# Optimization experiments

Measured on AMD Instinct MI355X. Metric: run time of the kernel, lower is better.

## Reference

```python
import jax, jax.numpy as jnp
import numpy as np

# Model dims
P_SPECS = [(6, 256), (7, 256)]          # pattern_length -> num_patterns (ordered)
P = 512                                  # total_num_patterns
MAXL = 7                                 # max_pattern_length
ND = 2                                   # num_diags (self-loop diag + main diag)
D = 300                                  # embedding_dim
V = 50000                                # vocab size
B = 32                                   # batch size
T = 128                                  # max_doc_len
NC = 2                                   # num_classes
NEG = -1e30                              # max-sum semiring zero; one = 0.0
END_STATES = np.concatenate([np.full(n, l - 1, dtype=np.int32) for l, n in P_SPECS])


def setup_inputs() -> dict:
    key = jax.random.key(0)
    ks = jax.random.split(key, 8)
    tokens = jax.random.randint(ks[0], (B, T), 0, V, dtype=jnp.int32)
    doc_lens = jax.random.randint(ks[1], (B,), 64, T + 1, dtype=jnp.int32)
    emb_table = jax.random.normal(ks[2], (V, D), dtype=jnp.float32)
    diags = jax.random.normal(ks[3], (P * ND * MAXL, D), dtype=jnp.float32)
    diags = diags / jnp.linalg.norm(diags, axis=1, keepdims=True)  # normalize(diags)
    bias = jax.random.normal(ks[4], (P * ND * MAXL, 1), dtype=jnp.float32)
    epsilons = jax.random.normal(ks[5], (P, MAXL - 1), dtype=jnp.float32)
    bn_weight = jnp.ones((P,), jnp.float32)
    bn_bias = jnp.zeros((P,), jnp.float32)
    final_w = 0.05 * jax.random.normal(ks[6], (NC, P), dtype=jnp.float32)
    final_b = jnp.zeros((NC,), jnp.float32)
    return dict(tokens=tokens, doc_lens=doc_lens, emb_table=emb_table, diags=diags,
                bias=bias, epsilons=epsilons, bn_weight=bn_weight, bn_bias=bn_bias,
                final_w=final_w, final_b=final_b)


def reference(tokens, doc_lens, emb_table, diags, bias, epsilons,
              bn_weight, bn_bias, final_w, final_b):
    # --- transition matrices (max-sum semiring: from_outer is identity) ---
    emb = emb_table[tokens]                                   # [B,T,D]
    # mm(diags, embeddings) + bias_scale * bias  (bias_scale = 1.0)
    ts = jnp.einsum('btd,kd->btk', emb, diags) + bias[:, 0]   # [B,T,P*ND*MAXL]
    ts = ts.reshape(B, T, P, ND, MAXL)                        # [B,T,P,ND,MAXL]

    end = jnp.asarray(END_STATES)                             # [P]
    hid0 = jnp.full((B, P, MAXL), NEG, jnp.float32).at[:, :, 0].set(0.0)
    sc0 = jnp.full((B, P), NEG, jnp.float32)                  # semiring.zero
    zpad = jnp.full((B, P, 1), NEG, jnp.float32)              # zero_padding
    rpad = jnp.zeros((B, P, 1), jnp.float32)                  # restart_padding (one)

    # epsilon_values = epsilon_scale (one=0) + epsilons
    def step(carry, xs):
        hid, sc = carry
        tm, i = xs                                            # tm: [B,P,ND,MAXL]
        # epsilon transitions
        ae = jnp.maximum(hid, jnp.concatenate([zpad, hid[:, :, :-1] + epsilons], axis=2))
        # main path: diag index -1 (the main diagonal)
        main = jnp.concatenate([rpad, ae[:, :, :-1] + tm[:, :, -1, :-1]], axis=2)
        # self loops: diag 0, self_loop_scale = semiring.one = 0
        sl = ae + tm[:, :, 0, :]
        hid = jnp.maximum(main, sl)
        endv = jnp.take_along_axis(hid, jnp.broadcast_to(end[None, :, None], (B, P, 1)), axis=2)[:, :, 0]
        sc = jnp.where((doc_lens > i)[:, None], jnp.maximum(sc, endv), sc)
        return (hid, sc), None

    (_, scores), _ = jax.lax.scan(step, (hid0, sc0),
                                  (jnp.moveaxis(ts, 1, 0), jnp.arange(T, dtype=jnp.int32)))

    # BatchNorm1d (training mode: biased batch statistics)
    mean = scores.mean(axis=0)
    var = scores.var(axis=0)
    scores = (scores - mean) * jax.lax.rsqrt(var + 1e-5) * bn_weight + bn_bias
    # binarize_scores
    scores = jnp.sign(jax.nn.relu(scores))
    # final linear layer
    return scores @ final_w.T + final_b                       # [B, NC]
```

## Files before the change

kernel.cpp:

```cpp
#include <hip/hip_runtime.h>

#define BB 32
#define TT 128
#define PP 512
#define DD 300
#define KT 10
#define NX 7168
#define AT 256
#define BT 448
#define NEG -1e30f

typedef _Float16 half8 __attribute__((ext_vector_type(8)));
typedef float floatx4 __attribute__((ext_vector_type(4)));

__device__ __forceinline__ void async_load16(const void* g, void* l) {
    __builtin_amdgcn_global_load_lds(
        (const __attribute__((address_space(1))) void*)g,
        (__attribute__((address_space(3))) void*)l, 16, 0, 0);
}

__device__ __forceinline__ floatx4 mfma16(half8 a, half8 b, floatx4 c) {
    return __builtin_amdgcn_mfma_f32_16x16x32_f16(a, b, c, 0, 0, 0);
}

__global__ __launch_bounds__(256) void pack_kernel(
    const int* __restrict__ tokens, const float* __restrict__ emb,
    const float* __restrict__ diags, const float* __restrict__ bias,
    _Float16* __restrict__ AhP, _Float16* __restrict__ AlP,
    _Float16* __restrict__ BhP, _Float16* __restrict__ BlP)
{
    const int idx = blockIdx.x * 256 + threadIdx.x;
    if (idx >= (AT + BT) * KT * 64) return;
    const int chunk = idx >> 6;
    const int ln = idx & 63;

    const float* src;
    float kslot;
    _Float16 *dh, *dl;
    int kt;
    if (chunk < AT * KT) {
        const int mt = chunk / KT; kt = chunk - mt * KT;
        const int m = mt * 16 + (ln & 15);
        src = emb + (size_t)tokens[m] * DD;
        kslot = 1.0f;
        dh = AhP + (size_t)chunk * 512 + ln * 8;
        dl = AlP + (size_t)chunk * 512 + ln * 8;
    } else {
        const int c2 = chunk - AT * KT;
        const int nt = c2 / KT; kt = c2 - nt * KT;
        const int n = nt * 16 + (ln & 15);
        src = diags + (size_t)n * DD;
        kslot = bias[n];
        dh = BhP + (size_t)c2 * 512 + ln * 8;
        dl = BlP + (size_t)c2 * 512 + ln * 8;
    }

    const int k0 = kt * 32 + (ln >> 4) * 8;
    float v[8];
    if (k0 + 8 <= DD) {
        float4 a = *(const float4*)(src + k0);
        float4 b = *(const float4*)(src + k0 + 4);
        v[0] = a.x; v[1] = a.y; v[2] = a.z; v[3] = a.w;
        v[4] = b.x; v[5] = b.y; v[6] = b.z; v[7] = b.w;
    } else {
        #pragma unroll
        for (int i = 0; i < 8; ++i) {
            const int k = k0 + i;
            v[i] = (k < DD) ? src[k] : (k == DD ? kslot : 0.f);
        }
    }
    half8 h, l;
    #pragma unroll
    for (int i = 0; i < 8; ++i) {
        h[i] = (_Float16)v[i];
        l[i] = (_Float16)((v[i] - (float)h[i]) * 4096.f);
    }
    *(half8*)dh = h;
    *(half8*)dl = l;
}

__global__ __launch_bounds__(256, 4) void gemm_kernel(
    const _Float16* __restrict__ AhP, const _Float16* __restrict__ AlP,
    const _Float16* __restrict__ BhP, const _Float16* __restrict__ BlP,
    const int* __restrict__ doc_lens,
    float* __restrict__ C)
{
    __shared__ __align__(16) _Float16 Bs[2][2][8][512];

    const int tid = threadIdx.x;
    const int w = tid >> 6, ln = tid & 63;
    const int n0t = blockIdx.x * 8, m0t = blockIdx.y * 4;
    const int wm = w & 1, wn = w >> 1;

    const int b  = blockIdx.y >> 1;
    const int th = blockIdx.y & 1;
    const int dl = doc_lens[b];
    if (th == 1 && dl <= 64) return;

    floatx4 acc0[2][4], acc1[2][4];
    #pragma unroll
    for (int i = 0; i < 2; ++i)
        #pragma unroll
        for (int j = 0; j < 4; ++j) {
            acc0[i][j] = (floatx4){0.f, 0.f, 0.f, 0.f};
            acc1[i][j] = (floatx4){0.f, 0.f, 0.f, 0.f};
        }

    half8 ah[2][2], al[2][2];

    auto loadA = [&](int kt, int pb) {
        #pragma unroll
        for (int i = 0; i < 2; ++i) {
            const size_t ch = ((size_t)(m0t + wm * 2 + i) * KT + kt) * 512 + ln * 8;
            ah[pb][i] = *(const half8*)(AhP + ch);
            al[pb][i] = *(const half8*)(AlP + ch);
        }
    };
    auto stageB = [&](int kt, int buf) {
        #pragma unroll
        for (int s = 0; s < 2; ++s) {
            const int nt = w + s * 4;
            const size_t ch = ((size_t)(n0t + nt) * KT + kt) * 512 + ln * 8;
            async_load16(BhP + ch, &Bs[buf][0][nt][0]);
            async_load16(BlP + ch, &Bs[buf][1][nt][0]);
        }
    };

    stageB(0, 0);
    loadA(0, 0);
    __syncthreads();

    #pragma unroll
    for (int kt = 0; kt < KT; ++kt) {
        const int cb = kt & 1, nb = cb ^ 1;
        if (kt + 1 < KT) {
            loadA(kt + 1, nb);
            stageB(kt + 1, nb);
        }
        #pragma unroll
        for (int j = 0; j < 4; ++j) {
            const half8 bh = *(const half8*)&Bs[cb][0][wn * 4 + j][ln * 8];
            const half8 bl = *(const half8*)&Bs[cb][1][wn * 4 + j][ln * 8];
            #pragma unroll
            for (int i = 0; i < 2; ++i) {
                acc0[i][j] = mfma16(ah[cb][i], bh, acc0[i][j]);
                acc1[i][j] = mfma16(ah[cb][i], bl, acc1[i][j]);
                acc1[i][j] = mfma16(al[cb][i], bh, acc1[i][j]);
            }
        }
        __syncthreads();
    }

    #pragma unroll
    for (int j = 0; j < 4; ++j) {
        const int n = (n0t + wn * 4 + j) * 16 + (ln & 15);
        #pragma unroll
        for (int i = 0; i < 2; ++i) {
            if (th * 64 + (wm * 2 + i) * 16 < dl) {
                const int mb = (m0t + wm * 2 + i) * 16 + (ln >> 4) * 4;
                #pragma unroll
                for (int r = 0; r < 4; ++r)
                    C[(size_t)(mb + r) * NX + n] =
                        acc0[i][j][r] + acc1[i][j][r] * (1.0f / 4096.0f);
            }
        }
    }
}

__global__ __launch_bounds__(64) void scan_kernel(
    const float* __restrict__ ts,
    const float* __restrict__ epsilons,
    const int* __restrict__ doc_lens,
    float* __restrict__ scores)
{
    const int b = blockIdx.x;
    const int p = blockIdx.y * 64 + threadIdx.x;
    const int dl = doc_lens[b];

    float e[6];
    #pragma unroll
    for (int i = 0; i < 6; ++i) e[i] = epsilons[p * 6 + i];

    const float* base = ts + (size_t)b * TT * NX + p * 14;

    float h0 = 0.f, h1 = NEG, h2 = NEG, h3 = NEG, h4 = NEG, h5 = NEG, h6 = NEG;
    float sc = NEG;
    const bool end5 = (p < 256);

    float2 buf[4][7];

    auto load = [&](int slot, int t) {
        const float2* s = (const float2*)(base + (size_t)t * NX);
        #pragma unroll
        for (int i = 0; i < 7; ++i) buf[slot][i] = s[i];
    };
    auto step = [&](int slot) {
        const float2* v = buf[slot];
        float ae0 = h0;
        float ae1 = fmaxf(h1, h0 + e[0]);
        float ae2 = fmaxf(h2, h1 + e[1]);
        float ae3 = fmaxf(h3, h2 + e[2]);
        float ae4 = fmaxf(h4, h3 + e[3]);
        float ae5 = fmaxf(h5, h4 + e[4]);
        float ae6 = fmaxf(h6, h5 + e[5]);
        h0 = fmaxf(0.f,            ae0 + v[0].x);
        h1 = fmaxf(ae0 + v[3].y,   ae1 + v[0].y);
        h2 = fmaxf(ae1 + v[4].x,   ae2 + v[1].x);
        h3 = fmaxf(ae2 + v[4].y,   ae3 + v[1].y);
        h4 = fmaxf(ae3 + v[5].x,   ae4 + v[2].x);
        h5 = fmaxf(ae4 + v[5].y,   ae5 + v[2].y);
        h6 = fmaxf(ae5 + v[6].x,   ae6 + v[3].x);
        sc = fmaxf(sc, end5 ? h5 : h6);
    };

    #pragma unroll
    for (int j = 0; j < 4; ++j) load(j, j);

    int tb = 0;
    for (; tb + 4 <= dl; tb += 4) {
        #pragma unroll
        for (int j = 0; j < 4; ++j) {
            step(j);
            const int t = tb + j + 4;
            load(j, t > 127 ? 127 : t);
        }
    }
    const int rem = dl - tb;
    #pragma unroll
    for (int j = 0; j < 3; ++j)
        if (j < rem) step(j);

    scores[p * BB + b] = sc;
}

__global__ __launch_bounds__(512) void finalize_kernel(
    const float* __restrict__ scores,
    const float* __restrict__ bn_w,
    const float* __restrict__ bn_b,
    const float* __restrict__ fw,
    const float* __restrict__ fb,
    float* __restrict__ out)
{
    __shared__ float acc[64];
    const int p = threadIdx.x;
    if (p < 64) acc[p] = 0.f;
    __syncthreads();

    float x[32];
    const float4* sp = (const float4*)(scores + p * 32);
    #pragma unroll
    for (int i = 0; i < 8; ++i) ((float4*)x)[i] = sp[i];

    float mean = 0.f;
    #pragma unroll
    for (int i = 0; i < 32; ++i) mean += x[i];
    mean *= (1.f / 32.f);
    float var = 0.f;
    #pragma unroll
    for (int i = 0; i < 32; ++i) { const float d = x[i] - mean; var = fmaf(d, d, var); }
    var *= (1.f / 32.f);

    const float scale = (1.f / sqrtf(var + 1e-5f)) * bn_w[p];
    const float shift = bn_b[p];
    const float w0 = fw[p], w1 = fw[PP + p];

    for (int b = 0; b < 32; ++b) {
        const float v = (x[b] - mean) * scale + shift;
        const bool bin = v > 0.f;
        float v0 = bin ? w0 : 0.f;
        float v1 = bin ? w1 : 0.f;
        #pragma unroll
        for (int o = 32; o; o >>= 1) {
            v0 += __shfl_xor(v0, o);
            v1 += __shfl_xor(v1, o);
        }
        if ((threadIdx.x & 63) == 0) {
            atomicAdd(&acc[b * 2 + 0], v0);
            atomicAdd(&acc[b * 2 + 1], v1);
        }
    }
    __syncthreads();
    if (p < 64) out[p] = acc[p] + fb[p & 1];
}

extern "C" void kernel_launch(void* const* d_in, const int* in_sizes, int n_in,
                              void* d_out, int out_size, void* d_ws, size_t ws_size,
                              hipStream_t stream) {
    const int*   tokens   = (const int*)d_in[0];
    const int*   doc_lens = (const int*)d_in[1];
    const float* emb      = (const float*)d_in[2];
    const float* diags    = (const float*)d_in[3];
    const float* bias     = (const float*)d_in[4];
    const float* eps      = (const float*)d_in[5];
    const float* bnw      = (const float*)d_in[6];
    const float* bnb      = (const float*)d_in[7];
    const float* fw       = (const float*)d_in[8];
    const float* fb       = (const float*)d_in[9];
    float* out = (float*)d_out;

    float* ts     = (float*)d_ws;
    float* scores = ts + (size_t)4096 * NX;
    _Float16* AhP = (_Float16*)(scores + PP * BB);
    _Float16* AlP = AhP + (size_t)AT * KT * 512;
    _Float16* BhP = AlP + (size_t)AT * KT * 512;
    _Float16* BlP = BhP + (size_t)BT * KT * 512;

    pack_kernel<<<(AT + BT) * KT * 64 / 256, 256, 0, stream>>>(
        tokens, emb, diags, bias, AhP, AlP, BhP, BlP);
    gemm_kernel<<<dim3(BT / 8, AT / 4), 256, 0, stream>>>(
        AhP, AlP, BhP, BlP, doc_lens, ts);
    scan_kernel<<<dim3(BB, PP / 64), 64, 0, stream>>>(ts, eps, doc_lens, scores);
    finalize_kernel<<<1, 512, 0, stream>>>(scores, bnw, bnb, fw, fb, out);
}
```

Measured before the change: 202.3 us.

## Switch split-fp16 GEMM to 32x32x16 MFMA tiles with repacked operands

Repacks the fp16 hi/lo operands into 32-row by 16-k chunks and rewrites the GEMM to use 32x32x16 MFMA instructions. Each wave now owns one 32-row token tile and four 32-column pattern tiles, one block per batch item. The goal is fewer MFMA issues and fewer LDS fragment reads per FLOP. In exchange, the per-half-document early exit is dropped, so rows past doc_len are computed but not stored, and occupancy hint drops to 2 blocks.

```diff
diff --git a/kernel.cpp b/kernel.cpp
--- a/kernel.cpp
+++ b/kernel.cpp
@@ -5,13 +5,14 @@
 #define PP 512
 #define DD 300
 #define KT 10
+#define KC 20
 #define NX 7168
-#define AT 256
-#define BT 448
+#define AT2 128
+#define BT2 224
 #define NEG -1e30f
 
 typedef _Float16 half8 __attribute__((ext_vector_type(8)));
-typedef float floatx4 __attribute__((ext_vector_type(4)));
+typedef float floatx16 __attribute__((ext_vector_type(16)));
 
 __device__ __forceinline__ void async_load16(const void* g, void* l) {
     __builtin_amdgcn_global_load_lds(
@@ -19,8 +20,8 @@
         (__attribute__((address_space(3))) void*)l, 16, 0, 0);
 }
 
-__device__ __forceinline__ floatx4 mfma16(half8 a, half8 b, floatx4 c) {
-    return __builtin_amdgcn_mfma_f32_16x16x32_f16(a, b, c, 0, 0, 0);
+__device__ __forceinline__ floatx16 mfma32(half8 a, half8 b, floatx16 c) {
+    return __builtin_amdgcn_mfma_f32_32x32x16_f16(a, b, c, 0, 0, 0);
 }
 
 __global__ __launch_bounds__(256) void pack_kernel(
@@ -30,32 +31,32 @@
     _Float16* __restrict__ BhP, _Float16* __restrict__ BlP)
 {
     const int idx = blockIdx.x * 256 + threadIdx.x;
-    if (idx >= (AT + BT) * KT * 64) return;
+    if (idx >= (AT2 + BT2) * KC * 64) return;
     const int chunk = idx >> 6;
     const int ln = idx & 63;
 
     const float* src;
     float kslot;
     _Float16 *dh, *dl;
-    int kt;
-    if (chunk < AT * KT) {
-        const int mt = chunk / KT; kt = chunk - mt * KT;
-        const int m = mt * 16 + (ln & 15);
+    int kc;
+    if (chunk < AT2 * KC) {
+        const int mt = chunk / KC; kc = chunk - mt * KC;
+        const int m = mt * 32 + (ln & 31);
         src = emb + (size_t)tokens[m] * DD;
         kslot = 1.0f;
         dh = AhP + (size_t)chunk * 512 + ln * 8;
         dl = AlP + (size_t)chunk * 512 + ln * 8;
     } else {
-        const int c2 = chunk - AT * KT;
-        const int nt = c2 / KT; kt = c2 - nt * KT;
-        const int n = nt * 16 + (ln & 15);
+        const int c2 = chunk - AT2 * KC;
+        const int nt = c2 / KC; kc = c2 - nt * KC;
+        const int n = nt * 32 + (ln & 31);
         src = diags + (size_t)n * DD;
         kslot = bias[n];
         dh = BhP + (size_t)c2 * 512 + ln * 8;
         dl = BlP + (size_t)c2 * 512 + ln * 8;
     }
 
-    const int k0 = kt * 32 + (ln >> 4) * 8;
+    const int k0 = kc * 16 + (ln >> 5) * 8;
     float v[8];
     if (k0 + 8 <= DD) {
         float4 a = *(const float4*)(src + k0);
@@ -79,50 +80,44 @@
     *(half8*)dl = l;
 }
 
-__global__ __launch_bounds__(256, 4) void gemm_kernel(
+__global__ __launch_bounds__(256, 2) void gemm_kernel(
     const _Float16* __restrict__ AhP, const _Float16* __restrict__ AlP,
     const _Float16* __restrict__ BhP, const _Float16* __restrict__ BlP,
     const int* __restrict__ doc_lens,
     float* __restrict__ C)
 {
-    __shared__ __align__(16) _Float16 Bs[2][2][8][512];
+    __shared__ __align__(16) _Float16 Bs[2][2][2][4][512];
 
     const int tid = threadIdx.x;
     const int w = tid >> 6, ln = tid & 63;
-    const int n0t = blockIdx.x * 8, m0t = blockIdx.y * 4;
-    const int wm = w & 1, wn = w >> 1;
-
-    const int b  = blockIdx.y >> 1;
-    const int th = blockIdx.y & 1;
+    const int n0t = blockIdx.x * 4;
+    const int b = blockIdx.y;
+    const int mtile = b * 4 + w;
     const int dl = doc_lens[b];
-    if (th == 1 && dl <= 64) return;
-
-    floatx4 acc0[2][4], acc1[2][4];
-    #pragma unroll
-    for (int i = 0; i < 2; ++i)
-        #pragma unroll
-        for (int j = 0; j < 4; ++j) {
-            acc0[i][j] = (floatx4){0.f, 0.f, 0.f, 0.f};
-            acc1[i][j] = (floatx4){0.f, 0.f, 0.f, 0.f};
-        }
+
+    floatx16 acc0[4], acc1[4];
+    #pragma unroll
+    for (int nt = 0; nt < 4; ++nt) {
+        #pragma unroll
+        for (int e = 0; e < 16; ++e) { acc0[nt][e] = 0.f; acc1[nt][e] = 0.f; }
+    }
 
     half8 ah[2][2], al[2][2];
 
     auto loadA = [&](int kt, int pb) {
         #pragma unroll
-        for (int i = 0; i < 2; ++i) {
-            const size_t ch = ((size_t)(m0t + wm * 2 + i) * KT + kt) * 512 + ln * 8;
-            ah[pb][i] = *(const half8*)(AhP + ch);
-            al[pb][i] = *(const half8*)(AlP + ch);
+        for (int q = 0; q < 2; ++q) {
+            const size_t ch = ((size_t)mtile * KC + 2 * kt + q) * 512 + ln * 8;
+            ah[pb][q] = *(const half8*)(AhP + ch);
+            al[pb][q] = *(const half8*)(AlP + ch);
         }
     };
+    const int sq = w & 1, shl = w >> 1;
     auto stageB = [&](int kt, int buf) {
         #pragma unroll
-        for (int s = 0; s < 2; ++s) {
-            const int nt = w + s * 4;
-            const size_t ch = ((size_t)(n0t + nt) * KT + kt) * 512 + ln * 8;
-            async_load16(BhP + ch, &Bs[buf][0][nt][0]);
-            async_load16(BlP + ch, &Bs[buf][1][nt][0]);
+        for (int s = 0; s < 4; ++s) {
+            const size_t ch = ((size_t)(n0t + s) * KC + 2 * kt + sq) * 512 + ln * 8;
+            async_load16((shl ? BlP : BhP) + ch, &Bs[buf][sq][shl][s][0]);
         }
     };
 
@@ -138,31 +133,31 @@
             stageB(kt + 1, nb);
         }
         #pragma unroll
-        for (int j = 0; j < 4; ++j) {
-            const half8 bh = *(const half8*)&Bs[cb][0][wn * 4 + j][ln * 8];
-            const half8 bl = *(const half8*)&Bs[cb][1][wn * 4 + j][ln * 8];
+        for (int nt = 0; nt < 4; ++nt) {
             #pragma unroll
-            for (int i = 0; i < 2; ++i) {
-                acc0[i][j] = mfma16(ah[cb][i], bh, acc0[i][j]);
-                acc1[i][j] = mfma16(ah[cb][i], bl, acc1[i][j]);
-                acc1[i][j] = mfma16(al[cb][i], bh, acc1[i][j]);
+            for (int q = 0; q < 2; ++q) {
+                const half8 bh = *(const half8*)&Bs[cb][q][0][nt][ln * 8];
+                const half8 bl = *(const half8*)&Bs[cb][q][1][nt][ln * 8];
+                acc0[nt] = mfma32(ah[cb][q], bh, acc0[nt]);
+                acc1[nt] = mfma32(ah[cb][q], bl, acc1[nt]);
+                acc1[nt] = mfma32(al[cb][q], bh, acc1[nt]);
             }
         }
         __syncthreads();
     }
 
-    #pragma unroll
-    for (int j = 0; j < 4; ++j) {
-        const int n = (n0t + wn * 4 + j) * 16 + (ln & 15);
-        #pragma unroll
-        for (int i = 0; i < 2; ++i) {
-            if (th * 64 + (wm * 2 + i) * 16 < dl) {
-                const int mb = (m0t + wm * 2 + i) * 16 + (ln >> 4) * 4;
-                #pragma unroll
-                for (int r = 0; r < 4; ++r)
-                    C[(size_t)(mb + r) * NX + n] =
-                        acc0[i][j][r] + acc1[i][j][r] * (1.0f / 4096.0f);
-            }
+    const int t0 = w * 32;
+    const int hi = (ln >> 5) * 4;
+    #pragma unroll
+    for (int nt = 0; nt < 4; ++nt) {
+        const int n = (n0t + nt) * 32 + (ln & 31);
+        #pragma unroll
+        for (int r = 0; r < 16; ++r) {
+            const int rl = (r & 3) + 8 * (r >> 2) + hi;
+            const int t = t0 + rl;
+            if (t < dl)
+                C[(size_t)(b * TT + t) * NX + n] =
+                    acc0[nt][r] + acc1[nt][r] * (1.0f / 4096.0f);
         }
     }
 }
@@ -301,13 +296,13 @@
     float* ts     = (float*)d_ws;
     float* scores = ts + (size_t)4096 * NX;
     _Float16* AhP = (_Float16*)(scores + PP * BB);
-    _Float16* AlP = AhP + (size_t)AT * KT * 512;
-    _Float16* BhP = AlP + (size_t)AT * KT * 512;
-    _Float16* BlP = BhP + (size_t)BT * KT * 512;
-
-    pack_kernel<<<(AT + BT) * KT * 64 / 256, 256, 0, stream>>>(
+    _Float16* AlP = AhP + (size_t)AT2 * KC * 512;
+    _Float16* BhP = AlP + (size_t)AT2 * KC * 512;
+    _Float16* BlP = BhP + (size_t)BT2 * KC * 512;
+
+    pack_kernel<<<(AT2 + BT2) * KC * 64 / 256, 256, 0, stream>>>(
         tokens, emb, diags, bias, AhP, AlP, BhP, BlP);
-    gemm_kernel<<<dim3(BT / 8, AT / 4), 256, 0, stream>>>(
+    gemm_kernel<<<dim3(BT2 / 4, BB), 256, 0, stream>>>(
         AhP, AlP, BhP, BlP, doc_lens, ts);
     scan_kernel<<<dim3(BB, PP / 64), 64, 0, stream>>>(ts, eps, doc_lens, scores);
     finalize_kernel<<<1, 512, 0, stream>>>(scores, bnw, bnb, fw, fb, out);
```

Result: slower. 207.8 us (+2.7%).

## Skip MFMAs on padded rows and fuse finalize into scan via last-block counter

Applied to the files above, without the earlier changes.

In the GEMM, the second half of each document's time range now issues MFMAs only for 16-row groups that fall within doc_len, so less tensor work is done on padding. The separate finalize kernel is removed: each scan block bumps a global atomic counter, and the last block to finish runs batch-norm, binarization and the final linear layer. The counter is reset in pack_kernel. This saves one kernel launch and some wasted MFMA work, but the whole finalize now runs serially in a single 64-thread wave that relies on atomics and threadfences.

```diff
diff --git a/kernel.cpp b/kernel.cpp
--- a/kernel.cpp
+++ b/kernel.cpp
@@ -27,9 +27,11 @@
     const int* __restrict__ tokens, const float* __restrict__ emb,
     const float* __restrict__ diags, const float* __restrict__ bias,
     _Float16* __restrict__ AhP, _Float16* __restrict__ AlP,
-    _Float16* __restrict__ BhP, _Float16* __restrict__ BlP)
+    _Float16* __restrict__ BhP, _Float16* __restrict__ BlP,
+    unsigned* __restrict__ done_cnt)
 {
     const int idx = blockIdx.x * 256 + threadIdx.x;
+    if (idx == 0) *done_cnt = 0u;
     if (idx >= (AT + BT) * KT * 64) return;
     const int chunk = idx >> 6;
     const int ln = idx & 63;
@@ -130,25 +132,55 @@
     loadA(0, 0);
     __syncthreads();
 
-    #pragma unroll
-    for (int kt = 0; kt < KT; ++kt) {
-        const int cb = kt & 1, nb = cb ^ 1;
-        if (kt + 1 < KT) {
-            loadA(kt + 1, nb);
-            stageB(kt + 1, nb);
-        }
-        #pragma unroll
-        for (int j = 0; j < 4; ++j) {
-            const half8 bh = *(const half8*)&Bs[cb][0][wn * 4 + j][ln * 8];
-            const half8 bl = *(const half8*)&Bs[cb][1][wn * 4 + j][ln * 8];
+    if (th == 0) {
+        #pragma unroll
+        for (int kt = 0; kt < KT; ++kt) {
+            const int cb = kt & 1, nb = cb ^ 1;
+            if (kt + 1 < KT) {
+                loadA(kt + 1, nb);
+                stageB(kt + 1, nb);
+            }
             #pragma unroll
-            for (int i = 0; i < 2; ++i) {
-                acc0[i][j] = mfma16(ah[cb][i], bh, acc0[i][j]);
-                acc1[i][j] = mfma16(ah[cb][i], bl, acc1[i][j]);
-                acc1[i][j] = mfma16(al[cb][i], bh, acc1[i][j]);
-            }
-        }
-        __syncthreads();
+            for (int j = 0; j < 4; ++j) {
+                const half8 bh = *(const half8*)&Bs[cb][0][wn * 4 + j][ln * 8];
+                const half8 bl = *(const half8*)&Bs[cb][1][wn * 4 + j][ln * 8];
+                #pragma unroll
+                for (int i = 0; i < 2; ++i) {
+                    acc0[i][j] = mfma16(ah[cb][i], bh, acc0[i][j]);
+                    acc1[i][j] = mfma16(ah[cb][i], bl, acc1[i][j]);
+                    acc1[i][j] = mfma16(al[cb][i], bh, acc1[i][j]);
+                }
+            }
+            __syncthreads();
+        }
+    } else {
+        const int nlive = ((dl - 64) + 15) >> 4;
+        const bool g0 = (wm * 2 + 0) < nlive;
+        const bool g1 = (wm * 2 + 1) < nlive;
+        #pragma unroll
+        for (int kt = 0; kt < KT; ++kt) {
+            const int cb = kt & 1, nb = cb ^ 1;
+            if (kt + 1 < KT) {
+                loadA(kt + 1, nb);
+                stageB(kt + 1, nb);
+            }
+            #pragma unroll
+            for (int j = 0; j < 4; ++j) {
+                const half8 bh = *(const half8*)&Bs[cb][0][wn * 4 + j][ln * 8];
+                const half8 bl = *(const half8*)&Bs[cb][1][wn * 4 + j][ln * 8];
+                if (g0) {
+                    acc0[0][j] = mfma16(ah[cb][0], bh, acc0[0][j]);
+                    acc1[0][j] = mfma16(ah[cb][0], bl, acc1[0][j]);
+                    acc1[0][j] = mfma16(al[cb][0], bh, acc1[0][j]);
+                }
+                if (g1) {
+                    acc0[1][j] = mfma16(ah[cb][1], bh, acc0[1][j]);
+                    acc1[1][j] = mfma16(ah[cb][1], bl, acc1[1][j]);
+                    acc1[1][j] = mfma16(al[cb][1], bh, acc1[1][j]);
+                }
+            }
+            __syncthreads();
+        }
     }
 
     #pragma unroll
@@ -171,7 +203,13 @@
     const float* __restrict__ ts,
     const float* __restrict__ epsilons,
     const int* __restrict__ doc_lens,
-    float* __restrict__ scores)
+    float* __restrict__ scores,
+    unsigned* __restrict__ done_cnt,
+    const float* __restrict__ bn_w,
+    const float* __restrict__ bn_b,
+    const float* __restrict__ fw,
+    const float* __restrict__ fb,
+    float* __restrict__ out)
 {
     const int b = blockIdx.x;
     const int p = blockIdx.y * 64 + threadIdx.x;
@@ -231,56 +269,62 @@
         if (j < rem) step(j);
 
     scores[p * BB + b] = sc;
-}
-
-__global__ __launch_bounds__(512) void finalize_kernel(
-    const float* __restrict__ scores,
-    const float* __restrict__ bn_w,
-    const float* __restrict__ bn_b,
-    const float* __restrict__ fw,
-    const float* __restrict__ fb,
-    float* __restrict__ out)
-{
-    __shared__ float acc[64];
-    const int p = threadIdx.x;
-    if (p < 64) acc[p] = 0.f;
+
     __syncthreads();
-
-    float x[32];
-    const float4* sp = (const float4*)(scores + p * 32);
-    #pragma unroll
-    for (int i = 0; i < 8; ++i) ((float4*)x)[i] = sp[i];
-
-    float mean = 0.f;
-    #pragma unroll
-    for (int i = 0; i < 32; ++i) mean += x[i];
-    mean *= (1.f / 32.f);
-    float var = 0.f;
-    #pragma unroll
-    for (int i = 0; i < 32; ++i) { const float d = x[i] - mean; var = fmaf(d, d, var); }
-    var *= (1.f / 32.f);
-
-    const float scale = (1.f / sqrtf(var + 1e-5f)) * bn_w[p];
-    const float shift = bn_b[p];
-    const float w0 = fw[p], w1 = fw[PP + p];
-
-    for (int b = 0; b < 32; ++b) {
-        const float v = (x[b] - mean) * scale + shift;
-        const bool bin = v > 0.f;
-        float v0 = bin ? w0 : 0.f;
-        float v1 = bin ? w1 : 0.f;
+    __threadfence();
+    int last = 0;
+    if (threadIdx.x == 0)
+        last = (atomicAdd(done_cnt, 1u) == (unsigned)(BB * (PP / 64)) - 1u);
+    last = __shfl(last, 0);
+    if (!last) return;
+    __threadfence();
+
+    const int t = threadIdx.x;
+    float s0[32], s1[32];
+    #pragma unroll
+    for (int i = 0; i < 32; ++i) { s0[i] = 0.f; s1[i] = 0.f; }
+
+    #pragma unroll
+    for (int pi = 0; pi < 8; ++pi) {
+        const int q = pi * 64 + t;
+        float x[32];
+        #pragma unroll
+        for (int i = 0; i < 32; ++i)
+            x[i] = __hip_atomic_load(&scores[q * 32 + i],
+                                     __ATOMIC_RELAXED, __HIP_MEMORY_SCOPE_AGENT);
+        float mean = 0.f;
+        #pragma unroll
+        for (int i = 0; i < 32; ++i) mean += x[i];
+        mean *= (1.f / 32.f);
+        float var = 0.f;
+        #pragma unroll
+        for (int i = 0; i < 32; ++i) { const float d = x[i] - mean; var = fmaf(d, d, var); }
+        var *= (1.f / 32.f);
+        const float scale = (1.f / sqrtf(var + 1e-5f)) * bn_w[q];
+        const float shift = bn_b[q];
+        const float w0 = fw[q], w1 = fw[PP + q];
+        #pragma unroll
+        for (int i = 0; i < 32; ++i) {
+            const float v = (x[i] - mean) * scale + shift;
+            if (v > 0.f) { s0[i] += w0; s1[i] += w1; }
+        }
+    }
+    #pragma unroll
+    for (int i = 0; i < 32; ++i) {
         #pragma unroll
         for (int o = 32; o; o >>= 1) {
-            v0 += __shfl_xor(v0, o);
-            v1 += __shfl_xor(v1, o);
-        }
-        if ((threadIdx.x & 63) == 0) {
-            atomicAdd(&acc[b * 2 + 0], v0);
-            atomicAdd(&acc[b * 2 + 1], v1);
-        }
-    }
-    __syncthreads();
-    if (p < 64) out[p] = acc[p] + fb[p & 1];
+            s0[i] += __shfl_xor(s0[i], o);
+            s1[i] += __shfl_xor(s1[i], o);
+        }
+    }
+    if (t == 0) {
+        const float b0 = fb[0], b1 = fb[1];
+        #pragma unroll
+        for (int i = 0; i < 32; ++i) {
+            out[2 * i]     = s0[i] + b0;
+            out[2 * i + 1] = s1[i] + b1;
+        }
+    }
 }
 
 extern "C" void kernel_launch(void* const* d_in, const int* in_sizes, int n_in,
@@ -298,17 +342,18 @@
     const float* fb       = (const float*)d_in[9];
     float* out = (float*)d_out;
 
-    float* ts     = (float*)d_ws;
-    float* scores = ts + (size_t)4096 * NX;
-    _Float16* AhP = (_Float16*)(scores + PP * BB);
+    float* ts       = (float*)d_ws;
+    float* scores   = ts + (size_t)4096 * NX;
+    unsigned* cnt   = (unsigned*)(scores + PP * BB);
+    _Float16* AhP   = (_Float16*)(scores + PP * BB + 16);
     _Float16* AlP = AhP + (size_t)AT * KT * 512;
     _Float16* BhP = AlP + (size_t)AT * KT * 512;
     _Float16* BlP = BhP + (size_t)BT * KT * 512;
 
     pack_kernel<<<(AT + BT) * KT * 64 / 256, 256, 0, stream>>>(
-        tokens, emb, diags, bias, AhP, AlP, BhP, BlP);
+        tokens, emb, diags, bias, AhP, AlP, BhP, BlP, cnt);
     gemm_kernel<<<dim3(BT / 8, AT / 4), 256, 0, stream>>>(
         AhP, AlP, BhP, BlP, doc_lens, ts);
-    scan_kernel<<<dim3(BB, PP / 64), 64, 0, stream>>>(ts, eps, doc_lens, scores);
-    finalize_kernel<<<1, 512, 0, stream>>>(scores, bnw, bnb, fw, fb, out);
-}
+    scan_kernel<<<dim3(BB, PP / 64), 64, 0, stream>>>(
+        ts, eps, doc_lens, scores, cnt, bnw, bnb, fw, fb, out);
+}
```

Result: slower. 257.5 us (+27.3%).
